# Performance work log

Hardware: AMD Instinct MI355X
Metric: run time of the kernel (lower is better)

Reference implementation:

```python
import jax, jax.numpy as jnp
import numpy as np

EPS = 1e-12  # matches torch F.normalize eps


def _l2_normalize(x):
    # F.normalize(x, p=2, dim=1): divide by clamped norm
    norm = jnp.sqrt(jnp.sum(x * x, axis=1, keepdims=True))
    return x / jnp.maximum(norm, EPS)


def setup_inputs() -> dict:
    key = jax.random.key(0)
    k1, k2, k3 = jax.random.split(key, 3)
    N, D, P, C = 16384, 768, 2048, 1000
    h = jax.random.normal(k1, (N, D), dtype=jnp.float32)
    prototypes = jax.random.normal(k2, (P, D), dtype=jnp.float32) * 0.1
    prototype_class = jax.random.normal(k3, (P, C), dtype=jnp.float32)
    temperature = jnp.float32(1.0)
    return {"h": h, "prototypes": prototypes,
            "prototype_class": prototype_class, "temperature": temperature}


def reference(h, prototypes, prototype_class, temperature):
    h_norm = _l2_normalize(h)                      # [N, D]
    p_norm = _l2_normalize(prototypes)             # [P, D]
    # cdist (p=2): sqrt(||a||^2 + ||b||^2 - 2 a.b), clamped at 0
    h_sq = jnp.sum(h_norm * h_norm, axis=1, keepdims=True)   # [N, 1]
    p_sq = jnp.sum(p_norm * p_norm, axis=1)                  # [P]
    dots = jnp.einsum('nd,pd->np', h_norm, p_norm)           # [N, P]
    dist_sq = jnp.maximum(h_sq + p_sq[None, :] - 2.0 * dots, 0.0)
    distances = jnp.sqrt(dist_sq)                            # [N, P]
    tau = jax.nn.softplus(temperature)
    activations = jnp.exp(-tau * distances)                  # [N, P]
    class_logits = jnp.matmul(activations, prototype_class)  # [N, C]
    return class_logits
```

## Files before the change

kernel.cpp:

```cpp
#include <hip/hip_runtime.h>
#include <hip/hip_bf16.h>
#include <math.h>

typedef unsigned short ushort_t;
typedef unsigned char uchar_t;
typedef unsigned int uint_t;
typedef __attribute__((ext_vector_type(8))) short bf16x8;
typedef __attribute__((ext_vector_type(4))) float f32x4;

#define AS1 __attribute__((address_space(1)))
#define AS3 __attribute__((address_space(3)))

__device__ __forceinline__ void gld_lds16(const void* g, void* l) {
  __builtin_amdgcn_global_load_lds((const AS1 void*)g, (AS3 void*)l, 16, 0, 0);
}

__device__ __forceinline__ ushort_t f32_to_bf16_bits(float v) {
  __hip_bfloat16 b = __float2bfloat16(v);
  return *(ushort_t*)&b;
}

__device__ __forceinline__ uint_t pack_fp8x4(float4 v, float sc) {
  int r = __builtin_amdgcn_cvt_pk_fp8_f32(v.x * sc, v.y * sc, 0, false);
  r = __builtin_amdgcn_cvt_pk_fp8_f32(v.z * sc, v.w * sc, r, true);
  return (uint_t)r;
}


__global__ __launch_bounds__(256) void prep(const float4* __restrict__ h,
                                            uchar_t* __restrict__ h8, int rowsH,
                                            const float4* __restrict__ p,
                                            uchar_t* __restrict__ p8, int rowsP,
                                            const float* __restrict__ pc,
                                            ushort_t* __restrict__ pcT,
                                            int P, int C, int normBlocks) {
  __shared__ float tile[32][33];
  if ((int)blockIdx.x < normBlocks) {
    int r = (blockIdx.x * 256 + threadIdx.x) >> 6;
    const int lane = threadIdx.x & 63;
    const float4* xr;
    uchar_t* o8;
    if (r < rowsH) {
      xr = h + (size_t)r * 192;
      o8 = h8;
    } else {
      r -= rowsH;
      if (r >= rowsP) return;
      xr = p + (size_t)r * 192;
      o8 = p8;
    }
    float4 v0 = xr[lane];
    float4 v1 = xr[lane + 64];
    float4 v2 = xr[lane + 128];
    float ss = v0.x * v0.x + v0.y * v0.y + v0.z * v0.z + v0.w * v0.w
             + v1.x * v1.x + v1.y * v1.y + v1.z * v1.z + v1.w * v1.w
             + v2.x * v2.x + v2.y * v2.y + v2.z * v2.z + v2.w * v2.w;
#pragma unroll
    for (int off = 32; off > 0; off >>= 1) ss += __shfl_xor(ss, off, 64);
    const float sc = 4.0f / fmaxf(sqrtf(ss), 1e-12f);
    const int rb = r >> 4, rl = r & 15;
    const int key = (rl >> 1) & 7;
    const int cc = (lane & 15) >> 1;
    const int cphys = ((cc ^ key) << 3) + ((lane & 1) << 2);
    const int ktb = lane >> 4;
    uchar_t* rowbase = o8 + (size_t)rb * 12 * 1024 + rl * 64 + cphys;
    *(uint_t*)(rowbase + (size_t)(ktb) * 1024)     = pack_fp8x4(v0, sc);
    *(uint_t*)(rowbase + (size_t)(4 + ktb) * 1024) = pack_fp8x4(v1, sc);
    *(uint_t*)(rowbase + (size_t)(8 + ktb) * 1024) = pack_fp8x4(v2, sc);
  } else {
    const int b = blockIdx.x - normBlocks;
    const int nkb = P / 32;
    const int bk = b % nkb, bc = b / nkb;
    const int k0 = bk * 32, c0 = bc * 32;
    const int tx = threadIdx.x & 31, ty = threadIdx.x >> 5;
#pragma unroll
    for (int rr = 0; rr < 4; ++rr) {
      const int c = c0 + tx;
      tile[ty + rr * 8][tx] = (c < C) ? pc[(size_t)(k0 + ty + rr * 8) * C + c] : 0.f;
    }
    __syncthreads();
    const int c2 = tx >> 3, off = tx & 7;
#pragma unroll
    for (int rr = 0; rr < 4; ++rr) {
      const int row = c0 + ty + rr * 8;
      const int rb = row >> 4, rl = row & 15;
      const int key4 = (rl >> 1) & 3;
      size_t us = (((size_t)rb * nkb + bk) * 16 + rl) * 32 + ((c2 ^ key4) << 3) + off;
      pcT[us] = f32_to_bf16_bits(tile[tx][ty + rr * 8]);
    }
  }
}

__launch_bounds__(256)
__global__ void gemm1_fp8(const uchar_t* __restrict__ A, const uchar_t* __restrict__ B,
                          ushort_t* __restrict__ act, const float* __restrict__ tptr,
                          int nKt, int actKT, int gx, int gxlog2) {
  __shared__ __align__(16) uchar_t As[16384];
  __shared__ __align__(16) uchar_t Bs[16384];
  const int tid = threadIdx.x, lane = tid & 63, wave = tid >> 6;
  const int wm = wave >> 1, wn = wave & 1;
  const int lid = blockIdx.x, xcd = lid & 7, q = lid >> 3;
  const int t = q & (gx - 1);
  const int s = ((q >> gxlog2) << 3) | xcd;

  f32x4 acc[4][4];
#pragma unroll
  for (int i = 0; i < 4; ++i)
#pragma unroll
    for (int j = 0; j < 4; ++j) acc[i][j] = (f32x4){0.f, 0.f, 0.f, 0.f};

  const uchar_t* aW = A + ((size_t)(s * 8 + 2 * wave) * nKt) * 1024 + lane * 16;
  const uchar_t* bW = B + ((size_t)(t * 8 + 2 * wave) * nKt) * 1024 + lane * 16;
  const size_t rstride = (size_t)nKt * 1024;
  uchar_t* lA = &As[wave * 4096];
  uchar_t* lB = &Bs[wave * 4096];

  const int fr = lane & 15, g = lane >> 4;
  const int key = (fr >> 1) & 7;
  const int rowoff = fr * 64;
  const int cp0 = ((g ^ key) << 3);
  const int cp1 = (((g | 4) ^ key) << 3);

  const int nIter = nKt >> 1;
  for (int kt = 0; kt < nIter; ++kt) {
    const size_t koff = (size_t)(2 * kt) * 1024;
    __syncthreads();
    gld_lds16(aW + koff, lA);
    gld_lds16(aW + koff + 1024, lA + 1024);
    gld_lds16(aW + rstride + koff, lA + 2048);
    gld_lds16(aW + rstride + koff + 1024, lA + 3072);
    gld_lds16(bW + koff, lB);
    gld_lds16(bW + koff + 1024, lB + 1024);
    gld_lds16(bW + rstride + koff, lB + 2048);
    gld_lds16(bW + rstride + koff + 1024, lB + 3072);
    __syncthreads();

#pragma unroll
    for (int kk = 0; kk < 2; ++kk) {
#pragma unroll
      for (int ksub = 0; ksub < 2; ++ksub) {
        const int cp = ksub ? cp1 : cp0;
        long a[4], b[4];
#pragma unroll
        for (int i = 0; i < 4; ++i)
          a[i] = *(const long*)&As[((wm * 4 + i) * 2 + kk) * 1024 + rowoff + cp];
#pragma unroll
        for (int j = 0; j < 4; ++j)
          b[j] = *(const long*)&Bs[((wn * 4 + j) * 2 + kk) * 1024 + rowoff + cp];
#pragma unroll
        for (int i = 0; i < 4; ++i)
#pragma unroll
          for (int j = 0; j < 4; ++j)
            acc[i][j] = __builtin_amdgcn_mfma_f32_16x16x32_fp8_fp8(a[i], b[j], acc[i][j], 0, 0, 0);
      }
    }
  }

  float tmp = *tptr;
  const float tau = log1pf(expf(tmp));
  const int crow = g * 4, ccol = fr;
  const int rowB = s * 128 + wm * 64, colB = t * 128 + wn * 64;
#pragma unroll
  for (int i = 0; i < 4; ++i)
#pragma unroll
    for (int j = 0; j < 4; ++j) {
      const int col = colB + j * 16 + ccol;
      const size_t ktile = col >> 5;
      const int c2 = (col >> 3) & 3, co = col & 7;
#pragma unroll
      for (int rr = 0; rr < 4; ++rr) {
        const int row = rowB + i * 16 + crow + rr;
        const int rb = row >> 4, rl = row & 15;
        const int key4 = (rl >> 1) & 3;
        float d2 = fmaxf(2.0f - acc[i][j][rr] * 0.125f, 0.0f);
        float d = d2 * rsqrtf(fmaxf(d2, 1e-20f));
        float a = __expf(-tau * d);
        act[(((size_t)rb * actKT + ktile) * 16 + rl) * 32 + ((c2 ^ key4) << 3) + co] =
            f32_to_bf16_bits(a);
      }
    }
}

#define BARRIER() do { asm volatile("" ::: "memory"); __builtin_amdgcn_s_barrier(); \
                       asm volatile("" ::: "memory"); } while (0)
#define LGKM0()   asm volatile("s_waitcnt lgkmcnt(0)" ::: "memory")
#define VM3()     asm volatile("s_waitcnt vmcnt(3)" ::: "memory")
#define VM0()     asm volatile("s_waitcnt vmcnt(0)" ::: "memory")
#define PRIO1()   __builtin_amdgcn_s_setprio(1)
#define PRIO0()   __builtin_amdgcn_s_setprio(0)
#define MM(a, b, c) __builtin_amdgcn_mfma_f32_16x16x32_bf16(a, b, c, 0, 0, 0)

__launch_bounds__(512, 4)
__global__ void gemm2_bf16_t3(const ushort_t* __restrict__ A,
                              const ushort_t* __restrict__ B,
                              float* __restrict__ out, int ldc, int ncols,
                              int nKt) {
  __shared__ __align__(16) uchar_t sm[73728];
  const int tid = threadIdx.x, lane = tid & 63, wave = tid >> 6;
  const int wm = wave >> 2, wn = wave & 3;
  const int lid = blockIdx.x, xcd = lid & 7, q = lid >> 3;
  const int tb = q & 3, sb = ((q >> 2) << 3) | xcd;

  f32x4 acc[4][4];
#pragma unroll
  for (int i = 0; i < 4; ++i)
#pragma unroll
    for (int j = 0; j < 4; ++j) acc[i][j] = (f32x4){0.f, 0.f, 0.f, 0.f};

  const uchar_t* Apl = (const uchar_t*)A + (((size_t)(sb * 8) * nKt) << 10) + lane * 16;
  const uchar_t* Bpl = (const uchar_t*)B + (((size_t)(tb * 16) * nKt) << 10) + lane * 16;

  const int fr = lane & 15, g = lane >> 4;
  const int rdoff = fr * 64 + ((g ^ ((fr >> 1) & 3)) << 4);
  const uchar_t* smA = sm + (wm << 12) + rdoff;
  const uchar_t* smB = sm + 8192 + (wn << 12) + rdoff;

#define T3_STA(r_, T_, bo_) gld_lds16(Apl + ((size_t)((r_) * nKt + (T_)) << 10), \
                                      sm + (bo_) + ((r_) << 10))
#define T3_STB(c_, T_, bo_) gld_lds16(Bpl + ((size_t)((c_) * nKt + (T_)) << 10), \
                                      sm + (bo_) + 8192 + ((c_) << 10))
#define T3_DSA(bo_, i_) (*(const bf16x8*)(smA + (bo_) + ((i_) << 10)))
#define T3_DSB(bo_, j_) (*(const bf16x8*)(smB + (bo_) + ((j_) << 10)))

  T3_STA(wave, 0, 0); T3_STB(wave, 0, 0); T3_STB(wave + 8, 0, 0);
  T3_STA(wave, 1, 24576); T3_STB(wave, 1, 24576); T3_STB(wave + 8, 1, 24576);
  VM3(); BARRIER();

  int boC = 0, boN = 24576, boNN = 49152;
  for (int kt = 0; kt < nKt; ++kt) {
    bf16x8 a0 = T3_DSA(boC, 0), a1 = T3_DSA(boC, 1), a2 = T3_DSA(boC, 2), a3 = T3_DSA(boC, 3);
    bf16x8 b0 = T3_DSB(boC, 0), b1 = T3_DSB(boC, 1), b2 = T3_DSB(boC, 2), b3 = T3_DSB(boC, 3);
    if (kt + 2 < nKt) {
      T3_STA(wave, kt + 2, boNN); T3_STB(wave, kt + 2, boNN); T3_STB(wave + 8, kt + 2, boNN);
    }
    BARRIER(); LGKM0();
    PRIO1();
    acc[0][0] = MM(a0, b0, acc[0][0]); acc[0][1] = MM(a0, b1, acc[0][1]);
    acc[0][2] = MM(a0, b2, acc[0][2]); acc[0][3] = MM(a0, b3, acc[0][3]);
    acc[1][0] = MM(a1, b0, acc[1][0]); acc[1][1] = MM(a1, b1, acc[1][1]);
    acc[1][2] = MM(a1, b2, acc[1][2]); acc[1][3] = MM(a1, b3, acc[1][3]);
    acc[2][0] = MM(a2, b0, acc[2][0]); acc[2][1] = MM(a2, b1, acc[2][1]);
    acc[2][2] = MM(a2, b2, acc[2][2]); acc[2][3] = MM(a2, b3, acc[2][3]);
    acc[3][0] = MM(a3, b0, acc[3][0]); acc[3][1] = MM(a3, b1, acc[3][1]);
    acc[3][2] = MM(a3, b2, acc[3][2]); acc[3][3] = MM(a3, b3, acc[3][3]);
    PRIO0();
    if (kt + 2 < nKt) { VM3(); } else if (kt + 1 < nKt) { VM0(); }
    BARRIER();
    int tswap = boC; boC = boN; boN = boNN; boNN = tswap;
  }

  const int crow = g * 4;
  const int rowB = sb * 128 + wm * 64, colB = tb * 256 + wn * 64;
#pragma unroll
  for (int i = 0; i < 4; ++i)
#pragma unroll
    for (int j = 0; j < 4; ++j) {
      const int col = colB + j * 16 + fr;
      if (col < ncols) {
#pragma unroll
        for (int rr = 0; rr < 4; ++rr)
          out[(size_t)(rowB + i * 16 + crow + rr) * ldc + col] = acc[i][j][rr];
      }
    }
}

extern "C" void kernel_launch(void* const* d_in, const int* in_sizes, int n_in,
                              void* d_out, int out_size, void* d_ws, size_t ws_size,
                              hipStream_t stream) {
  const float* h    = (const float*)d_in[0];
  const float* prot = (const float*)d_in[1];
  const float* pc   = (const float*)d_in[2];
  const float* temp = (const float*)d_in[3];
  float* out = (float*)d_out;

  const int D = 768;
  const int N = in_sizes[0] / D;
  const int P = in_sizes[1] / D;
  const int C = in_sizes[2] / P;
  const int CP = (C + 127) & ~127;

  char* ws = (char*)d_ws;
  size_t off = 0;
  uchar_t* h8   = (uchar_t*)(ws + off); off += (size_t)N * D;
  uchar_t* p8   = (uchar_t*)(ws + off); off += (size_t)P * D;
  ushort_t* pcT = (ushort_t*)(ws + off); off += (size_t)CP * P * 2;
  ushort_t* act = (ushort_t*)(ws + off); off += (size_t)N * P * 2;
  (void)ws_size;

  const int normBlocks = (N + P) / 4;
  const int transBlocks = (P / 32) * (CP / 32);
  prep<<<normBlocks + transBlocks, 256, 0, stream>>>(
      (const float4*)h, h8, N, (const float4*)prot, p8, P,
      pc, pcT, P, C, normBlocks);

  {
    const int GX = P / 128, GY = N / 128;
    gemm1_fp8<<<GX * GY, 256, 0, stream>>>(h8, p8, act, temp, D / 64, P / 32, GX, 4);
  }
  {
    const int GX = CP / 256, GY = N / 128;
    gemm2_bf16_t3<<<GX * GY, 512, 0, stream>>>(act, pcT, out, C, C, P / 32);
  }
}
```

Measured before the change: 217.0 us.

## Rewrite FP8 distance GEMM with 512-thread 128x256 tiles and triple-buffered LDS pipeline

Replaces the 256-thread 128x128 FP8 GEMM with a 512-thread 128x256 tile kernel that uses a triple-buffered LDS ring. Tile k+2 is prefetched while tile k is computed, with explicit vmcnt waits, barriers and raised wave priority around the MFMA block. The fp8 swizzle in the prep kernel changes so each lane reads 16 bytes per row and loads both k-halves in one LDS read. This targets the exposed global-load latency and synchronisation stalls of the old single-buffer loop, at the cost of much more LDS per block (72 KB), which may limit occupancy.

```diff
diff --git a/kernel.cpp b/kernel.cpp
--- a/kernel.cpp
+++ b/kernel.cpp
@@ -7,6 +7,7 @@
 typedef unsigned int uint_t;
 typedef __attribute__((ext_vector_type(8))) short bf16x8;
 typedef __attribute__((ext_vector_type(4))) float f32x4;
+typedef __attribute__((ext_vector_type(2))) long longx2;
 
 #define AS1 __attribute__((address_space(1)))
 #define AS3 __attribute__((address_space(3)))
@@ -59,9 +60,10 @@
     for (int off = 32; off > 0; off >>= 1) ss += __shfl_xor(ss, off, 64);
     const float sc = 4.0f / fmaxf(sqrtf(ss), 1e-12f);
     const int rb = r >> 4, rl = r & 15;
-    const int key = (rl >> 1) & 7;
-    const int cc = (lane & 15) >> 1;
-    const int cphys = ((cc ^ key) << 3) + ((lane & 1) << 2);
+    const int key4 = (rl >> 1) & 3;
+    const int u = (lane & 7) >> 1;
+    const int ksub = (lane & 15) >> 3;
+    const int cphys = ((u ^ key4) << 4) + (ksub << 3) + ((lane & 1) << 2);
     const int ktb = lane >> 4;
     uchar_t* rowbase = o8 + (size_t)rb * 12 * 1024 + rl * 64 + cphys;
     *(uint_t*)(rowbase + (size_t)(ktb) * 1024)     = pack_fp8x4(v0, sc);
@@ -91,17 +93,25 @@
   }
 }
 
-__launch_bounds__(256)
-__global__ void gemm1_fp8(const uchar_t* __restrict__ A, const uchar_t* __restrict__ B,
-                          ushort_t* __restrict__ act, const float* __restrict__ tptr,
-                          int nKt, int actKT, int gx, int gxlog2) {
-  __shared__ __align__(16) uchar_t As[16384];
-  __shared__ __align__(16) uchar_t Bs[16384];
+#define BARRIER() do { asm volatile("" ::: "memory"); __builtin_amdgcn_s_barrier(); \
+                       asm volatile("" ::: "memory"); } while (0)
+#define LGKM0()   asm volatile("s_waitcnt lgkmcnt(0)" ::: "memory")
+#define VM3()     asm volatile("s_waitcnt vmcnt(3)" ::: "memory")
+#define VM0()     asm volatile("s_waitcnt vmcnt(0)" ::: "memory")
+#define PRIO1()   __builtin_amdgcn_s_setprio(1)
+#define PRIO0()   __builtin_amdgcn_s_setprio(0)
+#define MM(a, b, c)  __builtin_amdgcn_mfma_f32_16x16x32_bf16(a, b, c, 0, 0, 0)
+#define MM8(a, b, c) __builtin_amdgcn_mfma_f32_16x16x32_fp8_fp8(a, b, c, 0, 0, 0)
+
+__launch_bounds__(512, 4)
+__global__ void gemm1_fp8_t3(const uchar_t* __restrict__ A, const uchar_t* __restrict__ B,
+                             ushort_t* __restrict__ act, const float* __restrict__ tptr,
+                             int nKt, int actKT, int gx, int gxlog2) {
+  __shared__ __align__(16) uchar_t sm1[73728];
   const int tid = threadIdx.x, lane = tid & 63, wave = tid >> 6;
-  const int wm = wave >> 1, wn = wave & 1;
+  const int wm = wave >> 2, wn = wave & 3;
   const int lid = blockIdx.x, xcd = lid & 7, q = lid >> 3;
-  const int t = q & (gx - 1);
-  const int s = ((q >> gxlog2) << 3) | xcd;
+  const int tb = q & (gx - 1), sb = ((q >> gxlog2) << 3) | xcd;
 
   f32x4 acc[4][4];
 #pragma unroll
@@ -109,62 +119,65 @@
 #pragma unroll
     for (int j = 0; j < 4; ++j) acc[i][j] = (f32x4){0.f, 0.f, 0.f, 0.f};
 
-  const uchar_t* aW = A + ((size_t)(s * 8 + 2 * wave) * nKt) * 1024 + lane * 16;
-  const uchar_t* bW = B + ((size_t)(t * 8 + 2 * wave) * nKt) * 1024 + lane * 16;
-  const size_t rstride = (size_t)nKt * 1024;
-  uchar_t* lA = &As[wave * 4096];
-  uchar_t* lB = &Bs[wave * 4096];
+  const uchar_t* Apl = A + (((size_t)(sb * 8) * nKt) << 10) + lane * 16;
+  const uchar_t* Bpl = B + (((size_t)(tb * 16) * nKt) << 10) + lane * 16;
 
   const int fr = lane & 15, g = lane >> 4;
-  const int key = (fr >> 1) & 7;
-  const int rowoff = fr * 64;
-  const int cp0 = ((g ^ key) << 3);
-  const int cp1 = (((g | 4) ^ key) << 3);
-
-  const int nIter = nKt >> 1;
-  for (int kt = 0; kt < nIter; ++kt) {
-    const size_t koff = (size_t)(2 * kt) * 1024;
-    __syncthreads();
-    gld_lds16(aW + koff, lA);
-    gld_lds16(aW + koff + 1024, lA + 1024);
-    gld_lds16(aW + rstride + koff, lA + 2048);
-    gld_lds16(aW + rstride + koff + 1024, lA + 3072);
-    gld_lds16(bW + koff, lB);
-    gld_lds16(bW + koff + 1024, lB + 1024);
-    gld_lds16(bW + rstride + koff, lB + 2048);
-    gld_lds16(bW + rstride + koff + 1024, lB + 3072);
-    __syncthreads();
-
-#pragma unroll
-    for (int kk = 0; kk < 2; ++kk) {
-#pragma unroll
-      for (int ksub = 0; ksub < 2; ++ksub) {
-        const int cp = ksub ? cp1 : cp0;
-        long a[4], b[4];
-#pragma unroll
-        for (int i = 0; i < 4; ++i)
-          a[i] = *(const long*)&As[((wm * 4 + i) * 2 + kk) * 1024 + rowoff + cp];
-#pragma unroll
-        for (int j = 0; j < 4; ++j)
-          b[j] = *(const long*)&Bs[((wn * 4 + j) * 2 + kk) * 1024 + rowoff + cp];
-#pragma unroll
-        for (int i = 0; i < 4; ++i)
-#pragma unroll
-          for (int j = 0; j < 4; ++j)
-            acc[i][j] = __builtin_amdgcn_mfma_f32_16x16x32_fp8_fp8(a[i], b[j], acc[i][j], 0, 0, 0);
-      }
-    }
+  const int rdoff = fr * 64 + ((g ^ ((fr >> 1) & 3)) << 4);
+  const uchar_t* smA = sm1 + (wm << 12) + rdoff;
+  const uchar_t* smB = sm1 + 8192 + (wn << 12) + rdoff;
+
+#define G1_STA(r_, T_, bo_) gld_lds16(Apl + ((size_t)((r_) * nKt + (T_)) << 10), \
+                                      sm1 + (bo_) + ((r_) << 10))
+#define G1_STB(c_, T_, bo_) gld_lds16(Bpl + ((size_t)((c_) * nKt + (T_)) << 10), \
+                                      sm1 + (bo_) + 8192 + ((c_) << 10))
+#define G1_DSA(bo_, i_) (*(const longx2*)(smA + (bo_) + ((i_) << 10)))
+#define G1_DSB(bo_, j_) (*(const longx2*)(smB + (bo_) + ((j_) << 10)))
+
+  G1_STA(wave, 0, 0); G1_STB(wave, 0, 0); G1_STB(wave + 8, 0, 0);
+  G1_STA(wave, 1, 24576); G1_STB(wave, 1, 24576); G1_STB(wave + 8, 1, 24576);
+  VM3(); BARRIER();
+
+  int boC = 0, boN = 24576, boNN = 49152;
+  for (int kt = 0; kt < nKt; ++kt) {
+    longx2 a0 = G1_DSA(boC, 0), a1 = G1_DSA(boC, 1), a2 = G1_DSA(boC, 2), a3 = G1_DSA(boC, 3);
+    longx2 b0 = G1_DSB(boC, 0), b1 = G1_DSB(boC, 1), b2 = G1_DSB(boC, 2), b3 = G1_DSB(boC, 3);
+    if (kt + 2 < nKt) {
+      G1_STA(wave, kt + 2, boNN); G1_STB(wave, kt + 2, boNN); G1_STB(wave + 8, kt + 2, boNN);
+    }
+    BARRIER(); LGKM0();
+    PRIO1();
+    acc[0][0] = MM8(a0[0], b0[0], acc[0][0]); acc[0][1] = MM8(a0[0], b1[0], acc[0][1]);
+    acc[0][2] = MM8(a0[0], b2[0], acc[0][2]); acc[0][3] = MM8(a0[0], b3[0], acc[0][3]);
+    acc[1][0] = MM8(a1[0], b0[0], acc[1][0]); acc[1][1] = MM8(a1[0], b1[0], acc[1][1]);
+    acc[1][2] = MM8(a1[0], b2[0], acc[1][2]); acc[1][3] = MM8(a1[0], b3[0], acc[1][3]);
+    acc[2][0] = MM8(a2[0], b0[0], acc[2][0]); acc[2][1] = MM8(a2[0], b1[0], acc[2][1]);
+    acc[2][2] = MM8(a2[0], b2[0], acc[2][2]); acc[2][3] = MM8(a2[0], b3[0], acc[2][3]);
+    acc[3][0] = MM8(a3[0], b0[0], acc[3][0]); acc[3][1] = MM8(a3[0], b1[0], acc[3][1]);
+    acc[3][2] = MM8(a3[0], b2[0], acc[3][2]); acc[3][3] = MM8(a3[0], b3[0], acc[3][3]);
+    acc[0][0] = MM8(a0[1], b0[1], acc[0][0]); acc[0][1] = MM8(a0[1], b1[1], acc[0][1]);
+    acc[0][2] = MM8(a0[1], b2[1], acc[0][2]); acc[0][3] = MM8(a0[1], b3[1], acc[0][3]);
+    acc[1][0] = MM8(a1[1], b0[1], acc[1][0]); acc[1][1] = MM8(a1[1], b1[1], acc[1][1]);
+    acc[1][2] = MM8(a1[1], b2[1], acc[1][2]); acc[1][3] = MM8(a1[1], b3[1], acc[1][3]);
+    acc[2][0] = MM8(a2[1], b0[1], acc[2][0]); acc[2][1] = MM8(a2[1], b1[1], acc[2][1]);
+    acc[2][2] = MM8(a2[1], b2[1], acc[2][2]); acc[2][3] = MM8(a2[1], b3[1], acc[2][3]);
+    acc[3][0] = MM8(a3[1], b0[1], acc[3][0]); acc[3][1] = MM8(a3[1], b1[1], acc[3][1]);
+    acc[3][2] = MM8(a3[1], b2[1], acc[3][2]); acc[3][3] = MM8(a3[1], b3[1], acc[3][3]);
+    PRIO0();
+    if (kt + 2 < nKt) { VM3(); } else if (kt + 1 < nKt) { VM0(); }
+    BARRIER();
+    int tswap = boC; boC = boN; boN = boNN; boNN = tswap;
   }
 
   float tmp = *tptr;
   const float tau = log1pf(expf(tmp));
-  const int crow = g * 4, ccol = fr;
-  const int rowB = s * 128 + wm * 64, colB = t * 128 + wn * 64;
+  const int crow = g * 4;
+  const int rowB = sb * 128 + wm * 64, colB = tb * 256 + wn * 64;
 #pragma unroll
   for (int i = 0; i < 4; ++i)
 #pragma unroll
     for (int j = 0; j < 4; ++j) {
-      const int col = colB + j * 16 + ccol;
+      const int col = colB + j * 16 + fr;
       const size_t ktile = col >> 5;
       const int c2 = (col >> 3) & 3, co = col & 7;
 #pragma unroll
@@ -180,15 +193,6 @@
       }
     }
 }
-
-#define BARRIER() do { asm volatile("" ::: "memory"); __builtin_amdgcn_s_barrier(); \
-                       asm volatile("" ::: "memory"); } while (0)
-#define LGKM0()   asm volatile("s_waitcnt lgkmcnt(0)" ::: "memory")
-#define VM3()     asm volatile("s_waitcnt vmcnt(3)" ::: "memory")
-#define VM0()     asm volatile("s_waitcnt vmcnt(0)" ::: "memory")
-#define PRIO1()   __builtin_amdgcn_s_setprio(1)
-#define PRIO0()   __builtin_amdgcn_s_setprio(0)
-#define MM(a, b, c) __builtin_amdgcn_mfma_f32_16x16x32_bf16(a, b, c, 0, 0, 0)
 
 __launch_bounds__(512, 4)
 __global__ void gemm2_bf16_t3(const ushort_t* __restrict__ A,
@@ -294,8 +298,8 @@
       pc, pcT, P, C, normBlocks);
 
   {
-    const int GX = P / 128, GY = N / 128;
-    gemm1_fp8<<<GX * GY, 256, 0, stream>>>(h8, p8, act, temp, D / 64, P / 32, GX, 4);
+    const int GX = P / 256, GY = N / 128;
+    gemm1_fp8_t3<<<GX * GY, 512, 0, stream>>>(h8, p8, act, temp, D / 64, P / 32, GX, 3);
   }
   {
     const int GX = CP / 256, GY = N / 128;
```

After: 214.2 us. About the same (-1.3%).
